# Performance work log

Measured on AMD Instinct MI355X. Metric: run time of the kernel, lower is better.

Reference implementation:

```python
import jax, jax.numpy as jnp
import numpy as np

B, S, I, H = 32, 1024, 256, 256
NUM_LAYERS = 2


def _lstm_dir(x, m, h0, c0, Wih, Whh, bih, bhh, reverse=False):
    """x: [S,B,in], m: [S,B,1]. Returns outs [S,B,H], hT, cT.
    PyTorch LSTMCell gate order: i, f, g, o. Masked reset to init state per step."""
    if reverse:
        x = x[::-1]
        m = m[::-1]

    def step(carry, xm):
        h, c = carry
        xt, mt = xm
        gates = xt @ Wih.T + bih + h @ Whh.T + bhh  # [B,4H]
        i, f, g, o = jnp.split(gates, 4, axis=-1)
        i = jax.nn.sigmoid(i)
        f = jax.nn.sigmoid(f)
        g = jnp.tanh(g)
        o = jax.nn.sigmoid(o)
        cn = f * c + i * g
        hn = o * jnp.tanh(cn)
        hn = hn * mt + h0 * (1.0 - mt)
        cn = cn * mt + c0 * (1.0 - mt)
        return (hn, cn), hn

    (hT, cT), outs = jax.lax.scan(step, (h0, c0), (x, m))
    if reverse:
        outs = outs[::-1]
    return outs, hT, cT


def setup_inputs() -> dict:
    key = jax.random.key(0)
    ks = iter(jax.random.split(key, 40))
    d = {
        "inputs": jax.random.normal(next(ks), (B, S, I), dtype=jnp.float32),
        "mask": jnp.ones((B, S), dtype=jnp.float32),
    }
    scale = 0.05
    for li in range(NUM_LAYERS):
        in_sz = I if li == 0 else 2 * H
        for d_tag in ("f", "b"):
            p = f"l{li}{d_tag}_"
            d[p + "Wih"] = jax.random.normal(next(ks), (4 * H, in_sz), dtype=jnp.float32) * scale
            d[p + "Whh"] = jax.random.normal(next(ks), (4 * H, H), dtype=jnp.float32) * scale
            d[p + "bih"] = jnp.zeros((4 * H,), dtype=jnp.float32)
            d[p + "bhh"] = jnp.zeros((4 * H,), dtype=jnp.float32)
    return d


def reference(inputs, mask,
              l0f_Wih, l0f_Whh, l0f_bih, l0f_bhh,
              l0b_Wih, l0b_Whh, l0b_bih, l0b_bhh,
              l1f_Wih, l1f_Whh, l1f_bih, l1f_bhh,
              l1b_Wih, l1b_Whh, l1b_bih, l1b_bhh):
    # batch_first -> time-major
    x = jnp.transpose(inputs, (1, 0, 2))          # [S,B,I]
    m = jnp.transpose(mask, (1, 0))[:, :, None]   # [S,B,1] broadcasts over H
    h0 = jnp.zeros((B, H), dtype=inputs.dtype)
    c0 = h0

    layers = [
        ((l0f_Wih, l0f_Whh, l0f_bih, l0f_bhh), (l0b_Wih, l0b_Whh, l0b_bih, l0b_bhh)),
        ((l1f_Wih, l1f_Whh, l1f_bih, l1f_bhh), (l1b_Wih, l1b_Whh, l1b_bih, l1b_bhh)),
    ]
    hn, cn = [], []
    for fw_p, bw_p in layers:
        # (dropout between layers only active in training mode; eval reference skips it)
        fw_out, fh, fc = _lstm_dir(x, m, h0, c0, *fw_p, reverse=False)
        bw_out, bh, bc = _lstm_dir(x, m, h0, c0, *bw_p, reverse=True)
        x = jnp.concatenate((fw_out, bw_out), axis=2)  # [S,B,2H]
        hn.append(jnp.concatenate((fh, bh), axis=1))
        cn.append(jnp.concatenate((fc, bc), axis=1))

    output = jnp.transpose(x, (1, 0, 2))  # [B,S,2H]
    return output, jnp.stack(hn, axis=0), jnp.stack(cn, axis=0)
```

## Files before the change

### kernel.cpp

```cpp
#include <hip/hip_runtime.h>
#include <cstddef>

typedef __attribute__((ext_vector_type(8))) short short8;
typedef __attribute__((ext_vector_type(4))) short short4v;
typedef __attribute__((ext_vector_type(4))) float f32x4;

__device__ __forceinline__ unsigned short f2bf(float f){
  unsigned u = __builtin_bit_cast(unsigned, f);
  u += 0x7FFFu + ((u >> 16) & 1u);
  return (unsigned short)(u >> 16);
}
__device__ __forceinline__ float bf2f(unsigned short h){
  unsigned u = ((unsigned)h) << 16;
  return __builtin_bit_cast(float, u);
}
__device__ __forceinline__ float sigf(float x){
  return __builtin_amdgcn_rcpf(1.0f + __builtin_amdgcn_exp2f(-1.4426950408889634f * x));
}
__device__ __forceinline__ float tanhf_(float x){
  return 1.0f - 2.0f * __builtin_amdgcn_rcpf(1.0f + __builtin_amdgcn_exp2f(2.8853900817779268f * x));
}

__global__ __launch_bounds__(64) void cast_x(const float* __restrict__ in, unsigned short* __restrict__ xb){
  int blk = blockIdx.x;
  int t = blk & 1023, b = blk >> 10;
  int k = threadIdx.x * 4;
  float4 v = *(const float4*)(in + (size_t)blk * 256 + k);
  unsigned lo = f2bf(v.x) | ((unsigned)f2bf(v.y) << 16);
  unsigned hi = f2bf(v.z) | ((unsigned)f2bf(v.w) << 16);
  *(uint2*)(xb + ((size_t)t * 32 + b) * 256 + k) = make_uint2(lo, hi);
}

__global__ __launch_bounds__(64) void cast_w(const float* __restrict__ Wf, const float* __restrict__ Wb,
    const float* __restrict__ bihf, const float* __restrict__ bhhf,
    const float* __restrict__ bihb, const float* __restrict__ bhhb,
    unsigned short* __restrict__ Bw, float* __restrict__ bias, int K){
  int row = blockIdx.x;
  int dd = row >> 10, gc = row & 1023;
  const float* src = (dd ? Wb : Wf) + (size_t)gc * K;
  unsigned short* dst = Bw + (size_t)row * K;
  for (int k = threadIdx.x * 4; k < K; k += 256){
    float4 v = *(const float4*)(src + k);
    unsigned lo = f2bf(v.x) | ((unsigned)f2bf(v.y) << 16);
    unsigned hi = f2bf(v.z) | ((unsigned)f2bf(v.w) << 16);
    *(uint2*)(dst + k) = make_uint2(lo, hi);
  }
  if (threadIdx.x == 0)
    bias[row] = dd ? (bihb[gc] + bhhb[gc]) : (bihf[gc] + bhhf[gc]);
}

__global__ __launch_bounds__(256) void gemm_xg(const unsigned short* __restrict__ A,
    const unsigned short* __restrict__ Bw, const float* __restrict__ bias,
    unsigned short* __restrict__ xg, int K){
  __shared__ __align__(16) unsigned short Al[128 * 64];
  __shared__ __align__(16) unsigned short Bl[128 * 64];
  const int tid = threadIdx.x;
  const int w = tid >> 6, l = tid & 63, q = l >> 4, cl = l & 15;
  const int bm = blockIdx.x >> 4, bn = blockIdx.x & 15;
  const int wm = w & 1, wn = w >> 1;
  f32x4 acc[4][4];
#pragma unroll
  for (int nt = 0; nt < 4; ++nt){
    float bv = bias[bn * 128 + wn * 64 + nt * 16 + cl];
#pragma unroll
    for (int mt = 0; mt < 4; ++mt) acc[mt][nt] = (f32x4){bv, bv, bv, bv};
  }
  const unsigned short* Ab = A + (size_t)(bm * 128) * K;
  const unsigned short* Bb = Bw + (size_t)(bn * 128) * K;
  for (int k0 = 0; k0 < K; k0 += 64){
#pragma unroll
    for (int i = 0; i < 4; ++i){
      int task = tid + i * 256;
      int row = task >> 3, ch = task & 7;
      int sw = ((ch ^ (row & 7)) * 8);
      *(uint4*)(&Al[row * 64 + sw]) = *(const uint4*)(Ab + (size_t)row * K + k0 + ch * 8);
      *(uint4*)(&Bl[row * 64 + sw]) = *(const uint4*)(Bb + (size_t)row * K + k0 + ch * 8);
    }
    __syncthreads();
#pragma unroll
    for (int kt2 = 0; kt2 < 2; ++kt2){
      short8 af[4], bfv[4];
#pragma unroll
      for (int mt = 0; mt < 4; ++mt){
        int row = wm * 64 + mt * 16 + cl;
        af[mt] = *(const short8*)(&Al[row * 64 + (((kt2 * 4 + q) ^ (row & 7)) * 8)]);
      }
#pragma unroll
      for (int nt = 0; nt < 4; ++nt){
        int n = wn * 64 + nt * 16 + cl;
        bfv[nt] = *(const short8*)(&Bl[n * 64 + (((kt2 * 4 + q) ^ (n & 7)) * 8)]);
      }
#pragma unroll
      for (int mt = 0; mt < 4; ++mt)
#pragma unroll
        for (int nt = 0; nt < 4; ++nt)
          acc[mt][nt] = __builtin_amdgcn_mfma_f32_16x16x32_bf16(af[mt], bfv[nt], acc[mt][nt], 0, 0, 0);
    }
    __syncthreads();
  }
#pragma unroll
  for (int mt = 0; mt < 4; ++mt){
    int row = bm * 128 + wm * 64 + mt * 16 + q * 4;
    int tt = row >> 5, bb = row & 31;
#pragma unroll
    for (int nt = 0; nt < 4; ++nt){
      int col = bn * 128 + wn * 64 + nt * 16 + cl;
      f32x4 v = acc[mt][nt];
      unsigned lo = f2bf(v[0]) | ((unsigned)f2bf(v[1]) << 16);
      unsigned hi = f2bf(v[2]) | ((unsigned)f2bf(v[3]) << 16);
      *(uint2*)(xg + ((size_t)tt * 2048 + col) * 32 + bb) = make_uint2(lo, hi);
    }
  }
}

__global__ __launch_bounds__(256, 1) void lstm_rec(const unsigned short* __restrict__ xg,
    const float* __restrict__ WhhF, const float* __restrict__ WhhB,
    const float* __restrict__ mask, unsigned* __restrict__ hx,
    unsigned short* __restrict__ houts, float* __restrict__ out,
    float* __restrict__ hnout, float* __restrict__ cnout, int layer){
  __shared__ __align__(16) unsigned short Abuf[2 * 8 * 8 * 40];
  __shared__ float maskL[8192];
  const int tid = threadIdx.x;
  const int w = tid >> 6, l = tid & 63, q = l >> 4, cl = l & 15;
  const int u = blockIdx.x & 7, s = blockIdx.x >> 3;
  const int d = u >> 2, b0 = (u & 3) * 8;
  const float* __restrict__ Whh = d ? WhhB : WhhF;
  const int jj = s * 64 + w * 16 + cl;
  short8 bfrag[4][8];
#pragma unroll
  for (int gi = 0; gi < 4; ++gi){
    const float* wr = Whh + (size_t)(gi * 256 + jj) * 256 + q * 8;
#pragma unroll
    for (int kt = 0; kt < 8; ++kt){
      float4 x0 = *(const float4*)(wr + kt * 32);
      float4 x1 = *(const float4*)(wr + kt * 32 + 4);
      short8 f;
      f[0] = (short)f2bf(x0.x); f[1] = (short)f2bf(x0.y); f[2] = (short)f2bf(x0.z); f[3] = (short)f2bf(x0.w);
      f[4] = (short)f2bf(x1.x); f[5] = (short)f2bf(x1.y); f[6] = (short)f2bf(x1.z); f[7] = (short)f2bf(x1.w);
      bfrag[gi][kt] = f;
    }
  }
  for (int idx = tid; idx < 8192; idx += 256){
    int tt = idx >> 3, r = idx & 7;
    maskL[idx] = mask[(size_t)(b0 + r) * 1024 + tt];
  }
  __syncthreads();
  float cst[4] = {0.f, 0.f, 0.f, 0.f};
  unsigned* hxu = hx + (size_t)u * 4096;
  const bool qv = (q < 2);
  const int bq = b0 + q * 4;
  const int row8 = cl & 7;
  for (int t = 0; t < 1024; ++t){
    const int ot = d ? (1023 - t) : t;
    const int par = t & 1;
    f32x4 acc[4];
    if (qv){
#pragma unroll
      for (int gi = 0; gi < 4; ++gi){
        const unsigned short* xp = xg + ((size_t)ot * 2048 + (d * 1024 + gi * 256 + jj)) * 32 + bq;
        short4v xv = *(const short4v*)xp;
        acc[gi] = (f32x4){bf2f((unsigned short)xv[0]), bf2f((unsigned short)xv[1]),
                          bf2f((unsigned short)xv[2]), bf2f((unsigned short)xv[3])};
      }
    } else {
#pragma unroll
      for (int gi = 0; gi < 4; ++gi) acc[gi] = (f32x4){0.f, 0.f, 0.f, 0.f};
    }
    if (t > 0 && cl < 8){
      const unsigned* base = hxu + (size_t)(par ^ 1) * 2048 + cl * 256 + q * 8;
      const uint4* p0 = (const uint4*)(base + w * 32);
      const uint4* p1 = p0 + 1;
      const uint4* p2 = (const uint4*)(base + (w + 4) * 32);
      const uint4* p3 = p2 + 1;
      const unsigned tagv = (unsigned)t;
      uint4 va, vb, vc, vd;
      while (true){
        asm volatile(
          "global_load_dwordx4 %0, %4, off sc1\n\t"
          "global_load_dwordx4 %1, %5, off sc1\n\t"
          "global_load_dwordx4 %2, %6, off sc1\n\t"
          "global_load_dwordx4 %3, %7, off sc1\n\t"
          "s_waitcnt vmcnt(0)"
          : "=v"(va), "=v"(vb), "=v"(vc), "=v"(vd)
          : "v"(p0), "v"(p1), "v"(p2), "v"(p3)
          : "memory");
        unsigned x = (va.x ^ tagv) | (va.y ^ tagv) | (va.z ^ tagv) | (va.w ^ tagv)
                   | (vb.x ^ tagv) | (vb.y ^ tagv) | (vb.z ^ tagv) | (vb.w ^ tagv)
                   | (vc.x ^ tagv) | (vc.y ^ tagv) | (vc.z ^ tagv) | (vc.w ^ tagv)
                   | (vd.x ^ tagv) | (vd.y ^ tagv) | (vd.z ^ tagv) | (vd.w ^ tagv);
        if (__all((x & 0xFFFFu) == 0u)) break;
      }
      unsigned short* dst = &Abuf[par * 2560 + w * 320 + cl * 40 + q * 8];
      *(uint4*)dst = (uint4){ (va.x >> 16) | (va.y & 0xFFFF0000u), (va.z >> 16) | (va.w & 0xFFFF0000u),
                              (vb.x >> 16) | (vb.y & 0xFFFF0000u), (vb.z >> 16) | (vb.w & 0xFFFF0000u) };
      unsigned short* dst2 = &Abuf[par * 2560 + (w + 4) * 320 + cl * 40 + q * 8];
      *(uint4*)dst2 = (uint4){ (vc.x >> 16) | (vc.y & 0xFFFF0000u), (vc.z >> 16) | (vc.w & 0xFFFF0000u),
                               (vd.x >> 16) | (vd.y & 0xFFFF0000u), (vd.z >> 16) | (vd.w & 0xFFFF0000u) };
    }
    __syncthreads();
    if (t > 0){
      short8 af[8];
#pragma unroll
      for (int kt = 0; kt < 8; ++kt)
        af[kt] = *(const short8*)(&Abuf[par * 2560 + kt * 320 + row8 * 40 + q * 8]);
#pragma unroll
      for (int kt = 0; kt < 8; ++kt)
#pragma unroll
        for (int gi = 0; gi < 4; ++gi)
          acc[gi] = __builtin_amdgcn_mfma_f32_16x16x32_bf16(af[kt], bfrag[gi][kt], acc[gi], 0, 0, 0);
    }
    if (qv){
      float hv[4];
      unsigned short hb[4];
#pragma unroll
      for (int r = 0; r < 4; ++r){
        float mvr = maskL[ot * 8 + q * 4 + r];
        float ig = sigf(acc[0][r]);
        float fg = sigf(acc[1][r]);
        float gg = tanhf_(acc[2][r]);
        float og = sigf(acc[3][r]);
        float cn = fg * cst[r] + ig * gg;
        float hn = og * tanhf_(cn);
        hn *= mvr; cn *= mvr;
        cst[r] = cn; hv[r] = hn; hb[r] = f2bf(hn);
      }
      const unsigned tagn = (unsigned)(t + 1);
      unsigned* sw = hxu + (size_t)par * 2048 + (size_t)(q * 4) * 256 + jj;
#pragma unroll
      for (int r = 0; r < 4; ++r)
        __hip_atomic_store(sw + r * 256, ((unsigned)hb[r] << 16) | tagn,
                           __ATOMIC_RELAXED, __HIP_MEMORY_SCOPE_AGENT);
      if (layer == 0){
#pragma unroll
        for (int r = 0; r < 4; ++r)
          houts[((size_t)ot * 32 + bq + r) * 512 + d * 256 + jj] = hb[r];
      } else {
#pragma unroll
        for (int r = 0; r < 4; ++r)
          out[((size_t)(bq + r) * 1024 + ot) * 512 + d * 256 + jj] = hv[r];
      }
      if (t == 1023){
#pragma unroll
        for (int r = 0; r < 4; ++r){
          size_t bo = (size_t)(layer * 32 + bq + r) * 512 + d * 256 + jj;
          hnout[bo] = hv[r];
          cnout[bo] = cst[r];
        }
      }
    }
  }
}

extern "C" void kernel_launch(void* const* d_in, const int* in_sizes, int n_in,
                              void* d_out, int out_size, void* d_ws, size_t ws_size,
                              hipStream_t stream){
  const float* inputs  = (const float*)d_in[0];
  const float* mask    = (const float*)d_in[1];
  const float* l0f_Wih = (const float*)d_in[2];
  const float* l0f_Whh = (const float*)d_in[3];
  const float* l0f_bih = (const float*)d_in[4];
  const float* l0f_bhh = (const float*)d_in[5];
  const float* l0b_Wih = (const float*)d_in[6];
  const float* l0b_Whh = (const float*)d_in[7];
  const float* l0b_bih = (const float*)d_in[8];
  const float* l0b_bhh = (const float*)d_in[9];
  const float* l1f_Wih = (const float*)d_in[10];
  const float* l1f_Whh = (const float*)d_in[11];
  const float* l1f_bih = (const float*)d_in[12];
  const float* l1f_bhh = (const float*)d_in[13];
  const float* l1b_Wih = (const float*)d_in[14];
  const float* l1b_Whh = (const float*)d_in[15];
  const float* l1b_bih = (const float*)d_in[16];
  const float* l1b_bhh = (const float*)d_in[17];

  char* ws = (char*)d_ws;
  unsigned short* xg   = (unsigned short*)(ws);
  unsigned short* xbf  = (unsigned short*)(ws + 134217728);
  unsigned short* hout = (unsigned short*)(ws + 150994944);
  unsigned short* B0   = (unsigned short*)(ws + 184549376);
  unsigned short* B1   = (unsigned short*)(ws + 185597952);
  float* bias0         = (float*)(ws + 187695104);
  float* bias1         = (float*)(ws + 187703296);
  unsigned* hx         = (unsigned*)(ws + 187711488);

  float* out   = (float*)d_out;
  float* hnout = out + 16777216;
  float* cnout = hnout + 32768;

  hipMemsetAsync(hx, 0, 262144, stream);
  cast_x<<<32768, 64, 0, stream>>>(inputs, xbf);
  cast_w<<<2048, 64, 0, stream>>>(l0f_Wih, l0b_Wih, l0f_bih, l0f_bhh, l0b_bih, l0b_bhh, B0, bias0, 256);
  cast_w<<<2048, 64, 0, stream>>>(l1f_Wih, l1b_Wih, l1f_bih, l1f_bhh, l1b_bih, l1b_bhh, B1, bias1, 512);
  gemm_xg<<<4096, 256, 0, stream>>>(xbf, B0, bias0, xg, 256);
  lstm_rec<<<32, 256, 0, stream>>>(xg, l0f_Whh, l0b_Whh, mask, hx, hout, nullptr, hnout, cnout, 0);
  gemm_xg<<<4096, 256, 0, stream>>>(hout, B1, bias1, xg, 512);
  lstm_rec<<<32, 256, 0, stream>>>(xg, l1f_Whh, l1b_Whh, mask, hx + 32768, nullptr, out, hnout, cnout, 1);
}
```

Before: 4.094 ms.

## Pair recurrent blocks so each handles half hidden units with local LDS exchange

The recurrent LSTM kernel is repartitioned from 32 blocks of 256 threads into 8 blocks of 512 threads. Each block owns 16 batch rows and half of the hidden units for one direction, so it exchanges only half of h through global memory with its partner block. Its own half goes through LDS, and those MFMAs are issued while the cross-block poll is still in flight. The next timestep's input-gate values are prefetched into registers. This cuts cross-block handshake traffic and the polling latency on the serial critical path, at the cost of fewer CUs in use and a more intricate spin-wait protocol.

```diff
diff --git a/kernel.cpp b/kernel.cpp
--- a/kernel.cpp
+++ b/kernel.cpp
@@ -113,141 +113,182 @@
   }
 }
 
-__global__ __launch_bounds__(256, 1) void lstm_rec(const unsigned short* __restrict__ xg,
+#define POLL8(EXTRA) \
+  asm volatile( \
+    "global_load_dwordx4 %0, %8, off sc1\n\t" \
+    "global_load_dwordx4 %1, %8, off offset:16 sc1\n\t" \
+    "global_load_dwordx4 %2, %8, off offset:128 sc1\n\t" \
+    "global_load_dwordx4 %3, %8, off offset:144 sc1\n\t" \
+    "global_load_dwordx4 %4, %8, off offset:256 sc1\n\t" \
+    "global_load_dwordx4 %5, %8, off offset:272 sc1\n\t" \
+    "global_load_dwordx4 %6, %8, off offset:384 sc1\n\t" \
+    "global_load_dwordx4 %7, %8, off offset:400 sc1" EXTRA \
+    : "=v"(pv0), "=v"(pv1), "=v"(pv2), "=v"(pv3), \
+      "=v"(pv4), "=v"(pv5), "=v"(pv6), "=v"(pv7) \
+    : "v"(pb) : "memory")
+
+#define CHK() ( \
+  xx = (pv0.x^tagv)|(pv0.y^tagv)|(pv0.z^tagv)|(pv0.w^tagv) \
+     | (pv1.x^tagv)|(pv1.y^tagv)|(pv1.z^tagv)|(pv1.w^tagv) \
+     | (pv2.x^tagv)|(pv2.y^tagv)|(pv2.z^tagv)|(pv2.w^tagv) \
+     | (pv3.x^tagv)|(pv3.y^tagv)|(pv3.z^tagv)|(pv3.w^tagv) \
+     | (pv4.x^tagv)|(pv4.y^tagv)|(pv4.z^tagv)|(pv4.w^tagv) \
+     | (pv5.x^tagv)|(pv5.y^tagv)|(pv5.z^tagv)|(pv5.w^tagv) \
+     | (pv6.x^tagv)|(pv6.y^tagv)|(pv6.z^tagv)|(pv6.w^tagv) \
+     | (pv7.x^tagv)|(pv7.y^tagv)|(pv7.z^tagv)|(pv7.w^tagv), \
+  __all((xx & 0xFFFFu) == 0u) )
+
+#define RKT(RT, UA, UB) { \
+  short8 ar; unsigned* arp = (unsigned*)&ar; \
+  arp[0] = __builtin_amdgcn_perm(UA.y, UA.x, 0x07060302u); \
+  arp[1] = __builtin_amdgcn_perm(UA.w, UA.z, 0x07060302u); \
+  arp[2] = __builtin_amdgcn_perm(UB.y, UB.x, 0x07060302u); \
+  arp[3] = __builtin_amdgcn_perm(UB.w, UB.z, 0x07060302u); \
+  acc[0] = __builtin_amdgcn_mfma_f32_16x16x32_bf16(ar, bfrag[0][4 + RT], acc[0], 0, 0, 0); \
+  acc[1] = __builtin_amdgcn_mfma_f32_16x16x32_bf16(ar, bfrag[1][4 + RT], acc[1], 0, 0, 0); \
+  acc[2] = __builtin_amdgcn_mfma_f32_16x16x32_bf16(ar, bfrag[2][4 + RT], acc[2], 0, 0, 0); \
+  acc[3] = __builtin_amdgcn_mfma_f32_16x16x32_bf16(ar, bfrag[3][4 + RT], acc[3], 0, 0, 0); }
+
+__global__ __launch_bounds__(512, 2) void lstm_rec(const unsigned short* __restrict__ xg,
     const float* __restrict__ WhhF, const float* __restrict__ WhhB,
     const float* __restrict__ mask, unsigned* __restrict__ hx,
     unsigned short* __restrict__ houts, float* __restrict__ out,
     float* __restrict__ hnout, float* __restrict__ cnout, int layer){
-  __shared__ __align__(16) unsigned short Abuf[2 * 8 * 8 * 40];
-  __shared__ float maskL[8192];
+  __shared__ __align__(16) unsigned short hbuf[2][16][136];
+  __shared__ __align__(16) float maskL[16384];
   const int tid = threadIdx.x;
   const int w = tid >> 6, l = tid & 63, q = l >> 4, cl = l & 15;
-  const int u = blockIdx.x & 7, s = blockIdx.x >> 3;
-  const int d = u >> 2, b0 = (u & 3) * 8;
+  const int bid = blockIdx.x;
+  const int ch = bid & 1, d = (bid >> 1) & 1, g = bid >> 2;
   const float* __restrict__ Whh = d ? WhhB : WhhF;
-  const int jj = s * 64 + w * 16 + cl;
+  const int jj = ch * 128 + w * 16 + cl;
+  const int ph = ch ^ 1;
+  const int ch4 = ch * 4, ph4 = ph * 4;
+
   short8 bfrag[4][8];
 #pragma unroll
   for (int gi = 0; gi < 4; ++gi){
-    const float* wr = Whh + (size_t)(gi * 256 + jj) * 256 + q * 8;
-#pragma unroll
-    for (int kt = 0; kt < 8; ++kt){
-      float4 x0 = *(const float4*)(wr + kt * 32);
-      float4 x1 = *(const float4*)(wr + kt * 32 + 4);
+    const float* wg = Whh + (size_t)(gi * 256 + jj) * 256 + q * 8;
+#pragma unroll
+    for (int p = 0; p < 8; ++p){
+      int gk = (p < 4) ? (ch4 + p) : (ph4 + (p - 4));
+      float4 x0 = *(const float4*)(wg + gk * 32);
+      float4 x1 = *(const float4*)(wg + gk * 32 + 4);
       short8 f;
       f[0] = (short)f2bf(x0.x); f[1] = (short)f2bf(x0.y); f[2] = (short)f2bf(x0.z); f[3] = (short)f2bf(x0.w);
       f[4] = (short)f2bf(x1.x); f[5] = (short)f2bf(x1.y); f[6] = (short)f2bf(x1.z); f[7] = (short)f2bf(x1.w);
-      bfrag[gi][kt] = f;
-    }
-  }
-  for (int idx = tid; idx < 8192; idx += 256){
-    int tt = idx >> 3, r = idx & 7;
-    maskL[idx] = mask[(size_t)(b0 + r) * 1024 + tt];
+      bfrag[gi][p] = f;
+    }
+  }
+  for (int i = tid; i < 16384; i += 512){
+    int tt = i >> 4, r = i & 15;
+    maskL[i] = mask[(size_t)(g * 16 + r) * 1024 + tt];
   }
   __syncthreads();
+
   float cst[4] = {0.f, 0.f, 0.f, 0.f};
-  unsigned* hxu = hx + (size_t)u * 4096;
-  const bool qv = (q < 2);
-  const int bq = b0 + q * 4;
-  const int row8 = cl & 7;
+  unsigned* hxu = hx + (size_t)(d * 2 + g) * 8192;
+  const unsigned* plA = hxu + cl * 256 + ph * 128 + q * 8;
+  const unsigned* plB = plA + 4096;
+  unsigned* stA = hxu + (q * 4) * 256 + jj;
+  unsigned* stB = stA + 4096;
+  const int bq = g * 16 + q * 4;
+  const size_t dj = (size_t)d * 256 + jj;
+  unsigned short* hob = houts + (size_t)bq * 512 + dj;
+  float* outb = out + (size_t)bq * 524288 + dj;
+
+  const ptrdiff_t tstep = d ? -65536 : 65536;
+  const unsigned short* xcur = xg + (size_t)(d ? 1023 : 0) * 65536
+                               + ((size_t)d * 1024 + jj) * 32 + g * 16 + q * 4;
+  short4v xp[4], xn[4];
+#pragma unroll
+  for (int gi = 0; gi < 4; ++gi) xp[gi] = *(const short4v*)(xcur + gi * 8192);
+
+#pragma unroll 2
   for (int t = 0; t < 1024; ++t){
+    const int par = t & 1;
     const int ot = d ? (1023 - t) : t;
-    const int par = t & 1;
     f32x4 acc[4];
-    if (qv){
-#pragma unroll
-      for (int gi = 0; gi < 4; ++gi){
-        const unsigned short* xp = xg + ((size_t)ot * 2048 + (d * 1024 + gi * 256 + jj)) * 32 + bq;
-        short4v xv = *(const short4v*)xp;
-        acc[gi] = (f32x4){bf2f((unsigned short)xv[0]), bf2f((unsigned short)xv[1]),
-                          bf2f((unsigned short)xv[2]), bf2f((unsigned short)xv[3])};
-      }
+#pragma unroll
+    for (int gi = 0; gi < 4; ++gi)
+      acc[gi] = (f32x4){bf2f((unsigned short)xp[gi][0]), bf2f((unsigned short)xp[gi][1]),
+                        bf2f((unsigned short)xp[gi][2]), bf2f((unsigned short)xp[gi][3])};
+    if (t > 0){
+      const unsigned* pb = par ? plA : plB;
+      uint4 pv0, pv1, pv2, pv3, pv4, pv5, pv6, pv7;
+      POLL8("");
+      const char* lbp = (const char*)(&hbuf[par ^ 1][0][0]) + cl * 272 + q * 16;
+#pragma unroll
+      for (int lt = 0; lt < 4; ++lt){
+        short8 a = *(const short8*)(lbp + lt * 64);
+        acc[0] = __builtin_amdgcn_mfma_f32_16x16x32_bf16(a, bfrag[0][lt], acc[0], 0, 0, 0);
+        acc[1] = __builtin_amdgcn_mfma_f32_16x16x32_bf16(a, bfrag[1][lt], acc[1], 0, 0, 0);
+        acc[2] = __builtin_amdgcn_mfma_f32_16x16x32_bf16(a, bfrag[2][lt], acc[2], 0, 0, 0);
+        acc[3] = __builtin_amdgcn_mfma_f32_16x16x32_bf16(a, bfrag[3][lt], acc[3], 0, 0, 0);
+      }
+      asm volatile("s_waitcnt vmcnt(0)" ::: "memory");
+      __builtin_amdgcn_sched_barrier(0);
+      const unsigned tagv = (unsigned)t;
+      unsigned xx;
+      if (!CHK()){
+        do{
+          POLL8("\n\ts_waitcnt vmcnt(0)");
+          __builtin_amdgcn_sched_barrier(0);
+        } while (!CHK());
+      }
+      if (t < 1023){
+#pragma unroll
+        for (int gi = 0; gi < 4; ++gi) xn[gi] = *(const short4v*)(xcur + tstep + gi * 8192);
+      }
+      RKT(0, pv0, pv1);
+      RKT(1, pv2, pv3);
+      RKT(2, pv4, pv5);
+      RKT(3, pv6, pv7);
     } else {
 #pragma unroll
-      for (int gi = 0; gi < 4; ++gi) acc[gi] = (f32x4){0.f, 0.f, 0.f, 0.f};
-    }
-    if (t > 0 && cl < 8){
-      const unsigned* base = hxu + (size_t)(par ^ 1) * 2048 + cl * 256 + q * 8;
-      const uint4* p0 = (const uint4*)(base + w * 32);
-      const uint4* p1 = p0 + 1;
-      const uint4* p2 = (const uint4*)(base + (w + 4) * 32);
-      const uint4* p3 = p2 + 1;
-      const unsigned tagv = (unsigned)t;
-      uint4 va, vb, vc, vd;
-      while (true){
-        asm volatile(
-          "global_load_dwordx4 %0, %4, off sc1\n\t"
-          "global_load_dwordx4 %1, %5, off sc1\n\t"
-          "global_load_dwordx4 %2, %6, off sc1\n\t"
-          "global_load_dwordx4 %3, %7, off sc1\n\t"
-          "s_waitcnt vmcnt(0)"
-          : "=v"(va), "=v"(vb), "=v"(vc), "=v"(vd)
-          : "v"(p0), "v"(p1), "v"(p2), "v"(p3)
-          : "memory");
-        unsigned x = (va.x ^ tagv) | (va.y ^ tagv) | (va.z ^ tagv) | (va.w ^ tagv)
-                   | (vb.x ^ tagv) | (vb.y ^ tagv) | (vb.z ^ tagv) | (vb.w ^ tagv)
-                   | (vc.x ^ tagv) | (vc.y ^ tagv) | (vc.z ^ tagv) | (vc.w ^ tagv)
-                   | (vd.x ^ tagv) | (vd.y ^ tagv) | (vd.z ^ tagv) | (vd.w ^ tagv);
-        if (__all((x & 0xFFFFu) == 0u)) break;
-      }
-      unsigned short* dst = &Abuf[par * 2560 + w * 320 + cl * 40 + q * 8];
-      *(uint4*)dst = (uint4){ (va.x >> 16) | (va.y & 0xFFFF0000u), (va.z >> 16) | (va.w & 0xFFFF0000u),
-                              (vb.x >> 16) | (vb.y & 0xFFFF0000u), (vb.z >> 16) | (vb.w & 0xFFFF0000u) };
-      unsigned short* dst2 = &Abuf[par * 2560 + (w + 4) * 320 + cl * 40 + q * 8];
-      *(uint4*)dst2 = (uint4){ (vc.x >> 16) | (vc.y & 0xFFFF0000u), (vc.z >> 16) | (vc.w & 0xFFFF0000u),
-                               (vd.x >> 16) | (vd.y & 0xFFFF0000u), (vd.z >> 16) | (vd.w & 0xFFFF0000u) };
+      for (int gi = 0; gi < 4; ++gi) xn[gi] = *(const short4v*)(xcur + tstep + gi * 8192);
+    }
+    f32x4 mv = *(const f32x4*)(&maskL[ot * 16 + q * 4]);
+    float hv[4]; unsigned short hb[4];
+#pragma unroll
+    for (int r = 0; r < 4; ++r){
+      float ig = sigf(acc[0][r]);
+      float fg = sigf(acc[1][r]);
+      float gg = tanhf_(acc[2][r]);
+      float og = sigf(acc[3][r]);
+      float cn = fg * cst[r] + ig * gg;
+      float hn = og * tanhf_(cn);
+      float m = mv[r];
+      hn *= m; cn *= m;
+      cst[r] = cn; hv[r] = hn; hb[r] = f2bf(hn);
+    }
+    unsigned* sw = par ? stB : stA;
+    const unsigned tagn = (unsigned)(t + 1);
+#pragma unroll
+    for (int r = 0; r < 4; ++r)
+      __hip_atomic_store(sw + r * 256, ((unsigned)hb[r] << 16) | tagn,
+                         __ATOMIC_RELAXED, __HIP_MEMORY_SCOPE_AGENT);
+#pragma unroll
+    for (int r = 0; r < 4; ++r) hbuf[par][q * 4 + r][w * 16 + cl] = hb[r];
+    if (layer == 0){
+#pragma unroll
+      for (int r = 0; r < 4; ++r) hob[(size_t)ot * 16384 + r * 512] = hb[r];
+    } else {
+#pragma unroll
+      for (int r = 0; r < 4; ++r) outb[(size_t)r * 524288 + (size_t)ot * 512] = hv[r];
+    }
+    if (t == 1023){
+#pragma unroll
+      for (int r = 0; r < 4; ++r){
+        size_t bo = (size_t)(layer * 32 + bq + r) * 512 + dj;
+        hnout[bo] = hv[r];
+        cnout[bo] = cst[r];
+      }
     }
     __syncthreads();
-    if (t > 0){
-      short8 af[8];
-#pragma unroll
-      for (int kt = 0; kt < 8; ++kt)
-        af[kt] = *(const short8*)(&Abuf[par * 2560 + kt * 320 + row8 * 40 + q * 8]);
-#pragma unroll
-      for (int kt = 0; kt < 8; ++kt)
-#pragma unroll
-        for (int gi = 0; gi < 4; ++gi)
-          acc[gi] = __builtin_amdgcn_mfma_f32_16x16x32_bf16(af[kt], bfrag[gi][kt], acc[gi], 0, 0, 0);
-    }
-    if (qv){
-      float hv[4];
-      unsigned short hb[4];
-#pragma unroll
-      for (int r = 0; r < 4; ++r){
-        float mvr = maskL[ot * 8 + q * 4 + r];
-        float ig = sigf(acc[0][r]);
-        float fg = sigf(acc[1][r]);
-        float gg = tanhf_(acc[2][r]);
-        float og = sigf(acc[3][r]);
-        float cn = fg * cst[r] + ig * gg;
-        float hn = og * tanhf_(cn);
-        hn *= mvr; cn *= mvr;
-        cst[r] = cn; hv[r] = hn; hb[r] = f2bf(hn);
-      }
-      const unsigned tagn = (unsigned)(t + 1);
-      unsigned* sw = hxu + (size_t)par * 2048 + (size_t)(q * 4) * 256 + jj;
-#pragma unroll
-      for (int r = 0; r < 4; ++r)
-        __hip_atomic_store(sw + r * 256, ((unsigned)hb[r] << 16) | tagn,
-                           __ATOMIC_RELAXED, __HIP_MEMORY_SCOPE_AGENT);
-      if (layer == 0){
-#pragma unroll
-        for (int r = 0; r < 4; ++r)
-          houts[((size_t)ot * 32 + bq + r) * 512 + d * 256 + jj] = hb[r];
-      } else {
-#pragma unroll
-        for (int r = 0; r < 4; ++r)
-          out[((size_t)(bq + r) * 1024 + ot) * 512 + d * 256 + jj] = hv[r];
-      }
-      if (t == 1023){
-#pragma unroll
-        for (int r = 0; r < 4; ++r){
-          size_t bo = (size_t)(layer * 32 + bq + r) * 512 + d * 256 + jj;
-          hnout[bo] = hv[r];
-          cnout[bo] = cst[r];
-        }
-      }
-    }
+#pragma unroll
+    for (int gi = 0; gi < 4; ++gi) xp[gi] = xn[gi];
+    xcur += tstep;
   }
 }
 
@@ -292,7 +333,7 @@
   cast_w<<<2048, 64, 0, stream>>>(l0f_Wih, l0b_Wih, l0f_bih, l0f_bhh, l0b_bih, l0b_bhh, B0, bias0, 256);
   cast_w<<<2048, 64, 0, stream>>>(l1f_Wih, l1b_Wih, l1f_bih, l1f_bhh, l1b_bih, l1b_bhh, B1, bias1, 512);
   gemm_xg<<<4096, 256, 0, stream>>>(xbf, B0, bias0, xg, 256);
-  lstm_rec<<<32, 256, 0, stream>>>(xg, l0f_Whh, l0b_Whh, mask, hx, hout, nullptr, hnout, cnout, 0);
+  lstm_rec<<<8, 512, 0, stream>>>(xg, l0f_Whh, l0b_Whh, mask, hx, hout, nullptr, hnout, cnout, 0);
   gemm_xg<<<4096, 256, 0, stream>>>(hout, B1, bias1, xg, 512);
-  lstm_rec<<<32, 256, 0, stream>>>(xg, l1f_Whh, l1b_Whh, mask, hx + 32768, nullptr, out, hnout, cnout, 1);
-}
+  lstm_rec<<<8, 512, 0, stream>>>(xg, l1f_Whh, l1b_Whh, mask, hx + 32768, nullptr, out, hnout, cnout, 1);
+}
```

After: 6.899 ms. 68.5% more time.
